# Kernel tuning notes

Measured on AMD Instinct MI355X. Metric: run time of the kernel, lower is better.

Reference implementation:

```python
import jax, jax.numpy as jnp
import numpy as np

B, C, H, W = 256, 3, 224, 224
RETINA = 32
NUM_ZOOM = 3
SCALE = 2
HG, HL = 1024, 256  # num_hidden_glimpse, num_hidden_location
GDIM = NUM_ZOOM * C * RETINA * RETINA  # 9216


def setup_inputs() -> dict:
    key = jax.random.key(0)
    ks = jax.random.split(key, 12)
    images = jax.random.normal(ks[0], (B, C, H, W), dtype=jnp.float32)
    # locations in [-0.4, 0.4] so all multi-scale crops are in-bounds
    locations = (jax.random.uniform(ks[1], (B, 2), dtype=jnp.float32) * 2.0 - 1.0) * 0.4
    def lin(kw, kb, fan_in, fan_out):
        s = 1.0 / np.sqrt(fan_in)
        Wm = jax.random.uniform(kw, (fan_in, fan_out), jnp.float32, -s, s)
        bm = jax.random.uniform(kb, (fan_out,), jnp.float32, -s, s)
        return Wm, bm
    W1, b1 = lin(ks[2], ks[3], GDIM, HG)
    W2, b2 = lin(ks[4], ks[5], 2, HL)
    W3, b3 = lin(ks[6], ks[7], HG, HG + HL)
    W4, b4 = lin(ks[8], ks[9], HL, HG + HL)
    return {"images": images, "locations": locations,
            "W1": W1, "b1": b1, "W2": W2, "b2": b2,
            "W3": W3, "b3": b3, "W4": W4, "b4": b4}


def _foveate(images, locations):
    # images (B,C,H,W); locations (B,2) in [-1,1]
    denorm = (locations + 1.0) * 0.5 * W  # denormalized pixel coords (row, col)
    zoom_patches = []
    for i in range(NUM_ZOOM):
        half = int(RETINA * 0.5 * SCALE ** i)
        size = 2 * half
        def crop(img, loc):
            # int() truncation == floor for in-bounds (non-negative) offsets
            top = jnp.trunc(loc[0] - half).astype(jnp.int32)
            left = jnp.trunc(loc[1] - half).astype(jnp.int32)
            return jax.lax.dynamic_slice(img, (jnp.int32(0), top, left), (C, size, size))
        crops = jax.vmap(crop)(images, denorm)  # (B,C,size,size)
        resized = jax.image.resize(crops, (crops.shape[0], C, RETINA, RETINA),
                                   method="bilinear", antialias=False)
        zoom_patches.append(resized)
    g = jnp.stack(zoom_patches, axis=1)  # (B, Z, C, r, r)
    return g.reshape(g.shape[0], -1)  # (B, Z*C*r*r)


def reference(images, locations, W1, b1, W2, b2, W3, b3, W4, b4):
    g = _foveate(images, locations)
    hg = jax.nn.relu(jax.nn.relu(g @ W1 + b1) @ W3 + b3)
    hl = jax.nn.relu(jax.nn.relu(locations @ W2 + b2) @ W4 + b4)
    return jax.nn.relu(hg + hl)
```

## Files before the change

### kernel.cpp

```cpp
#include <hip/hip_runtime.h>

typedef __attribute__((ext_vector_type(8))) short short8;
typedef __attribute__((ext_vector_type(4))) float f32x4;

#define Bsz 256
#define Cch 3
#define Him 224
#define Wim 224
#define RET 32
#define HG 1024
#define HL 256
#define GDIM 9216
#define NOUT 1280

__device__ __forceinline__ unsigned short f2bf(float x) {
  unsigned u = __float_as_uint(x);
  unsigned r = (u + 0x7fffu + ((u >> 16) & 1u)) >> 16;
  return (unsigned short)r;
}
__device__ __forceinline__ float bf2f(unsigned short h) {
  return __uint_as_float((unsigned)h << 16);
}

__global__ __launch_bounds__(256) void foveate_kernel(
    const float* __restrict__ img, const float* __restrict__ loc,
    unsigned short* __restrict__ ghi, unsigned short* __restrict__ glo) {
  int idx = blockIdx.x * 256 + threadIdx.x;
  int b = idx / GDIM;
  int r = idx - b * GDIM;
  int z = r / (Cch * RET * RET);
  int r2 = r - z * (Cch * RET * RET);
  int c = r2 / (RET * RET);
  int p = r2 - c * (RET * RET);
  int i = p >> 5, j = p & 31;
  float dr = (loc[b * 2 + 0] + 1.f) * .5f * (float)Wim;
  float dc = (loc[b * 2 + 1] + 1.f) * .5f * (float)Wim;
  int half = 16 << z;
  int top = (int)truncf(dr - (float)half), left = (int)truncf(dc - (float)half);
  const float* base = img + ((long)b * Cch + c) * (Him * Wim);
  float v;
  if (z == 0) {
    v = base[(top + i) * Wim + left + j];
  } else {
    int rr = (z == 1) ? top + 2 * i : top + 4 * i + 1;
    int cc = (z == 1) ? left + 2 * j : left + 4 * j + 1;
    v = .25f * (base[rr * Wim + cc] + base[rr * Wim + cc + 1] +
                base[(rr + 1) * Wim + cc] + base[(rr + 1) * Wim + cc + 1]);
  }
  unsigned short h = f2bf(v);
  ghi[idx] = h;
  glo[idx] = f2bf(v - bf2f(h));
}

__global__ __launch_bounds__(256) void tconv_kernel(
    const float* __restrict__ in, unsigned short* __restrict__ oh,
    unsigned short* __restrict__ ol, int K, int N) {
  __shared__ float tile[32][33];
  int n0 = blockIdx.x * 32, k0 = blockIdx.y * 32;
  int r = threadIdx.x >> 3, c4 = (threadIdx.x & 7) * 4;
  float4 v = *(const float4*)(in + (long)(k0 + r) * N + n0 + c4);
  tile[r][c4 + 0] = v.x; tile[r][c4 + 1] = v.y;
  tile[r][c4 + 2] = v.z; tile[r][c4 + 3] = v.w;
  __syncthreads();
  float x0 = tile[c4 + 0][r], x1 = tile[c4 + 1][r];
  float x2 = tile[c4 + 2][r], x3 = tile[c4 + 3][r];
  unsigned short h0 = f2bf(x0), h1 = f2bf(x1), h2 = f2bf(x2), h3 = f2bf(x3);
  long o = (long)(n0 + r) * K + k0 + c4;
  *(ushort4*)(oh + o) = make_ushort4(h0, h1, h2, h3);
  *(ushort4*)(ol + o) = make_ushort4(f2bf(x0 - bf2f(h0)), f2bf(x1 - bf2f(h1)),
                                     f2bf(x2 - bf2f(h2)), f2bf(x3 - bf2f(h3)));
}

__device__ __forceinline__ void mfma_tile(
    const unsigned short* __restrict__ Ahi, const unsigned short* __restrict__ Alo, int lda,
    const unsigned short* __restrict__ Bhi, const unsigned short* __restrict__ Blo, int ldb,
    int m0, int n0, int kb, int iters, f32x4 acc[4][4], unsigned short* lds) {
  const int t = threadIdx.x;
  const int lane = t & 63;
  const int wm = (t >> 7) & 1, wn = (t >> 6) & 1;
  unsigned short* pAh = lds;
  unsigned short* pAl = lds + 4096;
  unsigned short* pBh = lds + 8192;
  unsigned short* pBl = lds + 12288;
  const int c0 = t, c1 = t + 256;
  const int r0 = c0 >> 2, ko0 = c0 & 3;
  const int r1 = c1 >> 2, ko1 = c1 & 3;
  const long a0 = (long)(m0 + r0) * lda + kb + ko0 * 8;
  const long a1 = (long)(m0 + r1) * lda + kb + ko1 * 8;
  const long b0 = (long)(n0 + r0) * ldb + kb + ko0 * 8;
  const long b1 = (long)(n0 + r1) * ldb + kb + ko1 * 8;
  const int d0 = ((r0 >> 4) * 64 + (r0 & 15) + ko0 * 16) * 8;
  const int d1 = ((r1 >> 4) * 64 + (r1 & 15) + ko1 * 16) * 8;

  for (int it = 0; it < iters; ++it) {
    const long ka = (long)it * 32;
    uint4 vah0 = *(const uint4*)(Ahi + a0 + ka);
    uint4 vah1 = *(const uint4*)(Ahi + a1 + ka);
    uint4 val0 = *(const uint4*)(Alo + a0 + ka);
    uint4 val1 = *(const uint4*)(Alo + a1 + ka);
    uint4 vbh0 = *(const uint4*)(Bhi + b0 + ka);
    uint4 vbh1 = *(const uint4*)(Bhi + b1 + ka);
    uint4 vbl0 = *(const uint4*)(Blo + b0 + ka);
    uint4 vbl1 = *(const uint4*)(Blo + b1 + ka);
    __syncthreads();
    *(uint4*)(pAh + d0) = vah0; *(uint4*)(pAh + d1) = vah1;
    *(uint4*)(pAl + d0) = val0; *(uint4*)(pAl + d1) = val1;
    *(uint4*)(pBh + d0) = vbh0; *(uint4*)(pBh + d1) = vbh1;
    *(uint4*)(pBl + d0) = vbl0; *(uint4*)(pBl + d1) = vbl1;
    __syncthreads();
    short8 ah[4], al[4], bh[4], bl[4];
#pragma unroll
    for (int f = 0; f < 4; ++f) {
      int ra = ((wm * 4 + f) * 64 + lane) * 8;
      int rb = ((wn * 4 + f) * 64 + lane) * 8;
      ah[f] = *(const short8*)(pAh + ra);
      al[f] = *(const short8*)(pAl + ra);
      bh[f] = *(const short8*)(pBh + rb);
      bl[f] = *(const short8*)(pBl + rb);
    }
#pragma unroll
    for (int mf = 0; mf < 4; ++mf)
#pragma unroll
      for (int nf = 0; nf < 4; ++nf) {
        acc[mf][nf] = __builtin_amdgcn_mfma_f32_16x16x32_bf16(ah[mf], bh[nf], acc[mf][nf], 0, 0, 0);
        acc[mf][nf] = __builtin_amdgcn_mfma_f32_16x16x32_bf16(ah[mf], bl[nf], acc[mf][nf], 0, 0, 0);
        acc[mf][nf] = __builtin_amdgcn_mfma_f32_16x16x32_bf16(al[mf], bh[nf], acc[mf][nf], 0, 0, 0);
      }
  }
}

__device__ __forceinline__ void epilogue(float* __restrict__ Pz, int ldp, int m0, int n0,
                                         f32x4 acc[4][4]) {
  const int t = threadIdx.x, lane = t & 63;
  const int wm = (t >> 7) & 1, wn = (t >> 6) & 1;
  const int rbase = (lane >> 4) * 4, col = lane & 15;
#pragma unroll
  for (int mf = 0; mf < 4; ++mf)
#pragma unroll
    for (int nf = 0; nf < 4; ++nf) {
      int row = m0 + wm * 64 + mf * 16 + rbase;
      int cc = n0 + wn * 64 + nf * 16 + col;
#pragma unroll
      for (int r = 0; r < 4; ++r)
        Pz[(long)(row + r) * ldp + cc] = acc[mf][nf][r];
    }
}

__global__ __launch_bounds__(256, 2) void gemm1_kernel(
    const unsigned short* __restrict__ ghi, const unsigned short* __restrict__ glo,
    const unsigned short* __restrict__ w1thi, const unsigned short* __restrict__ w1tlo,
    float* __restrict__ P) {
  __shared__ __align__(16) unsigned short lds[16384];
  f32x4 zz = {0.f, 0.f, 0.f, 0.f};
  f32x4 acc[4][4];
  for (int i = 0; i < 4; ++i) for (int j = 0; j < 4; ++j) acc[i][j] = zz;
  int n0 = blockIdx.x * 128, m0 = blockIdx.y * 128, z = blockIdx.z;
  mfma_tile(ghi, glo, GDIM, w1thi, w1tlo, GDIM, m0, n0, z * 288, 9, acc, lds);
  epilogue(P + (long)z * Bsz * HG, HG, m0, n0, acc);
}

__global__ __launch_bounds__(256, 2) void gemm2_kernel(
    const unsigned short* __restrict__ h1hi, const unsigned short* __restrict__ h1lo,
    const unsigned short* __restrict__ h2hi, const unsigned short* __restrict__ h2lo,
    const unsigned short* __restrict__ w3thi, const unsigned short* __restrict__ w3tlo,
    const unsigned short* __restrict__ w4thi, const unsigned short* __restrict__ w4tlo,
    float* __restrict__ P) {
  __shared__ __align__(16) unsigned short lds[16384];
  f32x4 zz = {0.f, 0.f, 0.f, 0.f};
  f32x4 acc[4][4];
  for (int i = 0; i < 4; ++i) for (int j = 0; j < 4; ++j) acc[i][j] = zz;
  int n0 = blockIdx.x * 128, m0 = blockIdx.y * 128, z = blockIdx.z;
  if (z < 8)
    mfma_tile(h1hi, h1lo, HG, w3thi, w3tlo, HG, m0, n0, z * 128, 4, acc, lds);
  else
    mfma_tile(h2hi, h2lo, HL, w4thi, w4tlo, HL, m0, n0, 0, 8, acc, lds);
  epilogue(P + (long)z * Bsz * NOUT, NOUT, m0, n0, acc);
}

__global__ __launch_bounds__(256) void reduce1_kernel(
    const float* __restrict__ P, const float* __restrict__ b1,
    unsigned short* __restrict__ h1hi, unsigned short* __restrict__ h1lo) {
  int i4 = (blockIdx.x * 256 + threadIdx.x) * 4;
  float4 s = *(const float4*)(P + i4);
  for (int z = 1; z < 32; ++z) {
    float4 p = *(const float4*)(P + (long)z * (Bsz * HG) + i4);
    s.x += p.x; s.y += p.y; s.z += p.z; s.w += p.w;
  }
  int n = i4 & (HG - 1);
  float4 bb = *(const float4*)(b1 + n);
  float v0 = fmaxf(s.x + bb.x, 0.f), v1 = fmaxf(s.y + bb.y, 0.f);
  float v2 = fmaxf(s.z + bb.z, 0.f), v3 = fmaxf(s.w + bb.w, 0.f);
  unsigned short h0 = f2bf(v0), h1 = f2bf(v1), h2 = f2bf(v2), h3 = f2bf(v3);
  *(ushort4*)(h1hi + i4) = make_ushort4(h0, h1, h2, h3);
  *(ushort4*)(h1lo + i4) = make_ushort4(f2bf(v0 - bf2f(h0)), f2bf(v1 - bf2f(h1)),
                                        f2bf(v2 - bf2f(h2)), f2bf(v3 - bf2f(h3)));
}

__global__ __launch_bounds__(256) void h2_kernel(
    const float* __restrict__ loc, const float* __restrict__ W2,
    const float* __restrict__ b2, unsigned short* __restrict__ h2hi,
    unsigned short* __restrict__ h2lo) {
  int b = blockIdx.x, n = threadIdx.x;
  float s = fmaf(loc[b * 2], W2[n], fmaf(loc[b * 2 + 1], W2[HL + n], b2[n]));
  s = fmaxf(s, 0.f);
  unsigned short h = f2bf(s);
  h2hi[b * HL + n] = h;
  h2lo[b * HL + n] = f2bf(s - bf2f(h));
}

__global__ __launch_bounds__(256) void reduce2_kernel(
    const float* __restrict__ P, const float* __restrict__ b3,
    const float* __restrict__ b4, float* __restrict__ out) {
  int i4 = (blockIdx.x * 256 + threadIdx.x) * 4;
  float4 a = *(const float4*)(P + i4);
  for (int z = 1; z < 8; ++z) {
    float4 p = *(const float4*)(P + (long)z * (Bsz * NOUT) + i4);
    a.x += p.x; a.y += p.y; a.z += p.z; a.w += p.w;
  }
  float4 c = *(const float4*)(P + 8L * (Bsz * NOUT) + i4);
  int n = i4 % NOUT;
  float4 b3v = *(const float4*)(b3 + n);
  float4 b4v = *(const float4*)(b4 + n);
  float4 o;
  o.x = fmaxf(fmaxf(a.x + b3v.x, 0.f) + fmaxf(c.x + b4v.x, 0.f), 0.f);
  o.y = fmaxf(fmaxf(a.y + b3v.y, 0.f) + fmaxf(c.y + b4v.y, 0.f), 0.f);
  o.z = fmaxf(fmaxf(a.z + b3v.z, 0.f) + fmaxf(c.z + b4v.z, 0.f), 0.f);
  o.w = fmaxf(fmaxf(a.w + b3v.w, 0.f) + fmaxf(c.w + b4v.w, 0.f), 0.f);
  *(float4*)(out + i4) = o;
}

extern "C" void kernel_launch(void* const* d_in, const int* in_sizes, int n_in,
                              void* d_out, int out_size, void* d_ws, size_t ws_size,
                              hipStream_t stream) {
  const float* images = (const float*)d_in[0];
  const float* locs = (const float*)d_in[1];
  const float* W1 = (const float*)d_in[2];
  const float* b1 = (const float*)d_in[3];
  const float* W2 = (const float*)d_in[4];
  const float* b2 = (const float*)d_in[5];
  const float* W3 = (const float*)d_in[6];
  const float* b3 = (const float*)d_in[7];
  const float* W4 = (const float*)d_in[8];
  const float* b4 = (const float*)d_in[9];
  float* out = (float*)d_out;

  unsigned short* ghi = (unsigned short*)d_ws;
  unsigned short* glo = ghi + (long)Bsz * GDIM;
  unsigned short* w1thi = glo + (long)Bsz * GDIM;
  unsigned short* w1tlo = w1thi + (long)GDIM * HG;
  unsigned short* w3thi = w1tlo + (long)GDIM * HG;
  unsigned short* w3tlo = w3thi + (long)HG * NOUT;
  unsigned short* w4thi = w3tlo + (long)HG * NOUT;
  unsigned short* w4tlo = w4thi + (long)HL * NOUT;
  unsigned short* h1hi = w4tlo + (long)HL * NOUT;
  unsigned short* h1lo = h1hi + (long)Bsz * HG;
  unsigned short* h2hi = h1lo + (long)Bsz * HG;
  unsigned short* h2lo = h2hi + (long)Bsz * HL;
  float* P1 = (float*)(h2lo + (long)Bsz * HL);
  float* P2 = P1;

  tconv_kernel<<<dim3(HG / 32, GDIM / 32), 256, 0, stream>>>(W1, w1thi, w1tlo, GDIM, HG);
  tconv_kernel<<<dim3(NOUT / 32, HG / 32), 256, 0, stream>>>(W3, w3thi, w3tlo, HG, NOUT);
  tconv_kernel<<<dim3(NOUT / 32, HL / 32), 256, 0, stream>>>(W4, w4thi, w4tlo, HL, NOUT);
  foveate_kernel<<<(Bsz * GDIM) / 256, 256, 0, stream>>>(images, locs, ghi, glo);
  gemm1_kernel<<<dim3(HG / 128, Bsz / 128, 32), 256, 0, stream>>>(ghi, glo, w1thi, w1tlo, P1);
  reduce1_kernel<<<(Bsz * HG) / 1024, 256, 0, stream>>>(P1, b1, h1hi, h1lo);
  h2_kernel<<<Bsz, HL, 0, stream>>>(locs, W2, b2, h2hi, h2lo);
  gemm2_kernel<<<dim3(NOUT / 128, Bsz / 128, 9), 256, 0, stream>>>(
      h1hi, h1lo, h2hi, h2lo, w3thi, w3tlo, w4thi, w4tlo, P2);
  reduce2_kernel<<<(Bsz * NOUT) / 1024, 256, 0, stream>>>(P2, b3, b4, out);
}
```

Baseline: 298.8 us.

## Load GEMM tiles directly into LDS, vectorize foveation, split W4 GEMM across K

```diff
diff --git a/kernel.cpp b/kernel.cpp
--- a/kernel.cpp
+++ b/kernel.cpp
@@ -22,34 +22,49 @@
   return __uint_as_float((unsigned)h << 16);
 }
 
+#define GLL(gp, lp)                                                        \
+  __builtin_amdgcn_global_load_lds(                                        \
+      (const __attribute__((address_space(1))) unsigned int*)(gp),         \
+      (__attribute__((address_space(3))) unsigned int*)(lp), 16, 0, 0)
+
 __global__ __launch_bounds__(256) void foveate_kernel(
     const float* __restrict__ img, const float* __restrict__ loc,
     unsigned short* __restrict__ ghi, unsigned short* __restrict__ glo) {
-  int idx = blockIdx.x * 256 + threadIdx.x;
+  int q = blockIdx.x * 256 + threadIdx.x;
+  int idx = q * 4;
   int b = idx / GDIM;
   int r = idx - b * GDIM;
   int z = r / (Cch * RET * RET);
   int r2 = r - z * (Cch * RET * RET);
   int c = r2 / (RET * RET);
   int p = r2 - c * (RET * RET);
-  int i = p >> 5, j = p & 31;
+  int i = p >> 5, j0 = p & 31;
   float dr = (loc[b * 2 + 0] + 1.f) * .5f * (float)Wim;
   float dc = (loc[b * 2 + 1] + 1.f) * .5f * (float)Wim;
   int half = 16 << z;
   int top = (int)truncf(dr - (float)half), left = (int)truncf(dc - (float)half);
   const float* base = img + ((long)b * Cch + c) * (Him * Wim);
-  float v;
+  float v[4];
   if (z == 0) {
-    v = base[(top + i) * Wim + left + j];
+    const float* rp = base + (top + i) * Wim + left + j0;
+#pragma unroll
+    for (int t = 0; t < 4; ++t) v[t] = rp[t];
+  } else if (z == 1) {
+    const float* rp = base + (top + 2 * i) * Wim + left + 2 * j0;
+#pragma unroll
+    for (int t = 0; t < 4; ++t)
+      v[t] = .25f * (rp[2 * t] + rp[2 * t + 1] + rp[Wim + 2 * t] + rp[Wim + 2 * t + 1]);
   } else {
-    int rr = (z == 1) ? top + 2 * i : top + 4 * i + 1;
-    int cc = (z == 1) ? left + 2 * j : left + 4 * j + 1;
-    v = .25f * (base[rr * Wim + cc] + base[rr * Wim + cc + 1] +
-                base[(rr + 1) * Wim + cc] + base[(rr + 1) * Wim + cc + 1]);
-  }
-  unsigned short h = f2bf(v);
-  ghi[idx] = h;
-  glo[idx] = f2bf(v - bf2f(h));
+    const float* rp = base + (top + 4 * i + 1) * Wim + left + 4 * j0 + 1;
+#pragma unroll
+    for (int t = 0; t < 4; ++t)
+      v[t] = .25f * (rp[4 * t] + rp[4 * t + 1] + rp[Wim + 4 * t] + rp[Wim + 4 * t + 1]);
+  }
+  unsigned short h0 = f2bf(v[0]), h1 = f2bf(v[1]), h2 = f2bf(v[2]), h3 = f2bf(v[3]);
+  *(ushort4*)(ghi + idx) = make_ushort4(h0, h1, h2, h3);
+  *(ushort4*)(glo + idx) =
+      make_ushort4(f2bf(v[0] - bf2f(h0)), f2bf(v[1] - bf2f(h1)),
+                   f2bf(v[2] - bf2f(h2)), f2bf(v[3] - bf2f(h3)));
 }
 
 __global__ __launch_bounds__(256) void tconv_kernel(
@@ -77,36 +92,31 @@
     int m0, int n0, int kb, int iters, f32x4 acc[4][4], unsigned short* lds) {
   const int t = threadIdx.x;
   const int lane = t & 63;
+  const int wid = t >> 6;
   const int wm = (t >> 7) & 1, wn = (t >> 6) & 1;
   unsigned short* pAh = lds;
   unsigned short* pAl = lds + 4096;
   unsigned short* pBh = lds + 8192;
   unsigned short* pBl = lds + 12288;
-  const int c0 = t, c1 = t + 256;
-  const int r0 = c0 >> 2, ko0 = c0 & 3;
-  const int r1 = c1 >> 2, ko1 = c1 & 3;
-  const long a0 = (long)(m0 + r0) * lda + kb + ko0 * 8;
-  const long a1 = (long)(m0 + r1) * lda + kb + ko1 * 8;
-  const long b0 = (long)(n0 + r0) * ldb + kb + ko0 * 8;
-  const long b1 = (long)(n0 + r1) * ldb + kb + ko1 * 8;
-  const int d0 = ((r0 >> 4) * 64 + (r0 & 15) + ko0 * 16) * 8;
-  const int d1 = ((r1 >> 4) * 64 + (r1 & 15) + ko1 * 16) * 8;
+  const int c0 = 2 * wid, c1 = 2 * wid + 1;
+  const int sr = lane & 15, sk = (lane >> 4) * 8;
+  const long a0 = (long)(m0 + c0 * 16 + sr) * lda + kb + sk;
+  const long a1 = (long)(m0 + c1 * 16 + sr) * lda + kb + sk;
+  const long b0 = (long)(n0 + c0 * 16 + sr) * ldb + kb + sk;
+  const long b1 = (long)(n0 + c1 * 16 + sr) * ldb + kb + sk;
+  const int l0 = c0 * 512, l1 = c1 * 512;
 
   for (int it = 0; it < iters; ++it) {
     const long ka = (long)it * 32;
-    uint4 vah0 = *(const uint4*)(Ahi + a0 + ka);
-    uint4 vah1 = *(const uint4*)(Ahi + a1 + ka);
-    uint4 val0 = *(const uint4*)(Alo + a0 + ka);
-    uint4 val1 = *(const uint4*)(Alo + a1 + ka);
-    uint4 vbh0 = *(const uint4*)(Bhi + b0 + ka);
-    uint4 vbh1 = *(const uint4*)(Bhi + b1 + ka);
-    uint4 vbl0 = *(const uint4*)(Blo + b0 + ka);
-    uint4 vbl1 = *(const uint4*)(Blo + b1 + ka);
     __syncthreads();
-    *(uint4*)(pAh + d0) = vah0; *(uint4*)(pAh + d1) = vah1;
-    *(uint4*)(pAl + d0) = val0; *(uint4*)(pAl + d1) = val1;
-    *(uint4*)(pBh + d0) = vbh0; *(uint4*)(pBh + d1) = vbh1;
-    *(uint4*)(pBl + d0) = vbl0; *(uint4*)(pBl + d1) = vbl1;
+    GLL(Ahi + a0 + ka, pAh + l0);
+    GLL(Ahi + a1 + ka, pAh + l1);
+    GLL(Alo + a0 + ka, pAl + l0);
+    GLL(Alo + a1 + ka, pAl + l1);
+    GLL(Bhi + b0 + ka, pBh + l0);
+    GLL(Bhi + b1 + ka, pBh + l1);
+    GLL(Blo + b0 + ka, pBl + l0);
+    GLL(Blo + b1 + ka, pBl + l1);
     __syncthreads();
     short8 ah[4], al[4], bh[4], bl[4];
 #pragma unroll
@@ -173,7 +183,7 @@
   if (z < 8)
     mfma_tile(h1hi, h1lo, HG, w3thi, w3tlo, HG, m0, n0, z * 128, 4, acc, lds);
   else
-    mfma_tile(h2hi, h2lo, HL, w4thi, w4tlo, HL, m0, n0, 0, 8, acc, lds);
+    mfma_tile(h2hi, h2lo, HL, w4thi, w4tlo, HL, m0, n0, (z - 8) * 128, 4, acc, lds);
   epilogue(P + (long)z * Bsz * NOUT, NOUT, m0, n0, acc);
 }
 
@@ -217,7 +227,10 @@
     float4 p = *(const float4*)(P + (long)z * (Bsz * NOUT) + i4);
     a.x += p.x; a.y += p.y; a.z += p.z; a.w += p.w;
   }
-  float4 c = *(const float4*)(P + 8L * (Bsz * NOUT) + i4);
+  float4 c0 = *(const float4*)(P + 8L * (Bsz * NOUT) + i4);
+  float4 c1 = *(const float4*)(P + 9L * (Bsz * NOUT) + i4);
+  float4 c;
+  c.x = c0.x + c1.x; c.y = c0.y + c1.y; c.z = c0.z + c1.z; c.w = c0.w + c1.w;
   int n = i4 % NOUT;
   float4 b3v = *(const float4*)(b3 + n);
   float4 b4v = *(const float4*)(b4 + n);
@@ -262,11 +275,11 @@
   tconv_kernel<<<dim3(HG / 32, GDIM / 32), 256, 0, stream>>>(W1, w1thi, w1tlo, GDIM, HG);
   tconv_kernel<<<dim3(NOUT / 32, HG / 32), 256, 0, stream>>>(W3, w3thi, w3tlo, HG, NOUT);
   tconv_kernel<<<dim3(NOUT / 32, HL / 32), 256, 0, stream>>>(W4, w4thi, w4tlo, HL, NOUT);
-  foveate_kernel<<<(Bsz * GDIM) / 256, 256, 0, stream>>>(images, locs, ghi, glo);
+  foveate_kernel<<<(Bsz * GDIM) / 1024, 256, 0, stream>>>(images, locs, ghi, glo);
   gemm1_kernel<<<dim3(HG / 128, Bsz / 128, 32), 256, 0, stream>>>(ghi, glo, w1thi, w1tlo, P1);
   reduce1_kernel<<<(Bsz * HG) / 1024, 256, 0, stream>>>(P1, b1, h1hi, h1lo);
   h2_kernel<<<Bsz, HL, 0, stream>>>(locs, W2, b2, h2hi, h2lo);
-  gemm2_kernel<<<dim3(NOUT / 128, Bsz / 128, 9), 256, 0, stream>>>(
+  gemm2_kernel<<<dim3(NOUT / 128, Bsz / 128, 10), 256, 0, stream>>>(
       h1hi, h1lo, h2hi, h2lo, w3thi, w3tlo, w4thi, w4tlo, P2);
   reduce2_kernel<<<(Bsz * NOUT) / 1024, 256, 0, stream>>>(P2, b3, b4, out);
 }
```

New measurement: 295.7 us. About the same (-1.0%).
